# Performance work log

Measured on AMD Instinct MI355X. Metric: run time of the kernel, lower is better.

## Reference

```python
import jax, jax.numpy as jnp
import numpy as np

LAMBDA_SPATIAL = 1.0  # fixed buffer, not trained
GAMMA_ADJ = 1.0       # fixed buffer, not trained


def setup_inputs() -> dict:
    key = jax.random.key(0)
    k1, k2, k3, k4 = jax.random.split(key, 4)
    B, T, N, D = 8, 20, 512, 64
    h = jax.random.normal(k1, (B, T, N, D), dtype=jnp.float32)
    velocities = jax.random.normal(k2, (B, T, N, 2), dtype=jnp.float32)
    adjacency_weighted = jax.random.uniform(k3, (B, T, N, N), dtype=jnp.float32)
    node_mask = jax.random.randint(k4, (B, T, N), 0, 2).astype(bool)
    return {
        "h": h,
        "velocities": velocities,
        "adjacency_weighted": adjacency_weighted,
        "node_mask": node_mask,
    }


def reference(h, velocities, adjacency_weighted, node_mask):
    # h: [B,T,N,d]; velocities: [B,T,N,2]; adjacency_weighted: [B,T,N,N]; node_mask: [B,T,N]
    mask = node_mask.astype(bool)
    pair_m = mask[..., :, None] & mask[..., None, :]          # [B,T,N,N]

    # pairwise squared velocity distance, Eq. (3)
    dv = velocities[..., :, None, :] - velocities[..., None, :, :]  # [B,T,N,N,2]
    d2 = jnp.maximum(jnp.sum(dv * dv, axis=-1), 0.0)                # [B,T,N,N]

    logits_s = -LAMBDA_SPATIAL * d2 + GAMMA_ADJ * adjacency_weighted
    neg = jnp.finfo(logits_s.dtype).min
    logits_s = jnp.where(pair_m, logits_s, neg)
    row_ok = mask[..., :, None]
    logits_s = jnp.where(row_ok, logits_s, jnp.zeros_like(logits_s))

    alpha = jax.nn.softmax(logits_s, axis=-1)
    alpha = jnp.nan_to_num(alpha, nan=0.0, posinf=0.0, neginf=0.0)
    alpha = alpha / jnp.maximum(jnp.sum(alpha, axis=-1, keepdims=True), 1e-8)
    h_spatial = jnp.matmul(alpha, h)                          # [B,T,N,d]

    # temporal path: masked mean-pool over nodes, T x T similarity softmax
    mask_f = mask.astype(h.dtype)
    denom = jnp.maximum(jnp.sum(mask_f, axis=-1, keepdims=True), 1.0)  # [B,T,1]
    h_mean = jnp.sum(h * mask_f[..., None], axis=-2) / denom           # [B,T,d]
    m_b = jnp.matmul(h_mean, jnp.swapaxes(h_mean, -1, -2))             # [B,T,T]
    beta = jax.nn.softmax(m_b, axis=-1)
    h_temporal = jnp.einsum("btu,bund->btnd", beta, h)                 # [B,T,N,d]

    out = (h + h_spatial + h_temporal) * mask_f[..., None]
    return out
```

## Files before the change

kernel.cpp:

```cpp
#include <hip/hip_runtime.h>
#include <float.h>

#define BB 8
#define TT 20
#define NN 512
#define DD 64
#define BT (BB*TT)

typedef __bf16 bf16x8 __attribute__((ext_vector_type(8)));
typedef __bf16 bf16x4 __attribute__((ext_vector_type(4)));
typedef float f32x4 __attribute__((ext_vector_type(4)));

__global__ __launch_bounds__(256) void kpre(const float* __restrict__ h,
                                            const float* __restrict__ vel,
                                            const int* __restrict__ mask,
                                            __bf16* __restrict__ ht,
                                            __bf16* __restrict__ hb16,
                                            float* __restrict__ hpart,
                                            int* __restrict__ cpart,
                                            float4* __restrict__ colinfo,
                                            int* __restrict__ rows) {
    int bx = blockIdx.x;
    int bt = bx >> 3, slice = bx & 7;
    int n0 = slice * 64;
    int tid = threadIdx.x;
    const float* hp = h + ((size_t)bt * NN + n0) * DD;
    const int* mp = mask + (size_t)bt * NN + n0;
    short* htp = (short*)(ht + (size_t)bt * DD * NN) + n0;

    __shared__ __bf16 t[64][72];
    __shared__ float sred[16][64];

    int d4 = (tid & 15) << 2;
    int nl0 = tid >> 4;
    float s0 = 0.f, s1 = 0.f, s2 = 0.f, s3 = 0.f;
#pragma unroll
    for (int it = 0; it < 4; ++it) {
        int nl = it * 16 + nl0;
        float4 v = *(const float4*)(hp + (size_t)nl * DD + d4);
        if (mp[nl]) { s0 += v.x; s1 += v.y; s2 += v.z; s3 += v.w; }
        __bf16 b0 = (__bf16)v.x, b1 = (__bf16)v.y, b2 = (__bf16)v.z, b3 = (__bf16)v.w;
        t[d4 + 0][nl] = b0;
        t[d4 + 1][nl] = b1;
        t[d4 + 2][nl] = b2;
        t[d4 + 3][nl] = b3;
        bf16x4 pv = {b0, b1, b2, b3};
        *(bf16x4*)(hb16 + ((size_t)bt * NN + n0 + nl) * DD + d4) = pv;
    }
    int g = tid >> 4;
    sred[g][d4 + 0] = s0; sred[g][d4 + 1] = s1;
    sred[g][d4 + 2] = s2; sred[g][d4 + 3] = s3;
    __syncthreads();
#pragma unroll
    for (int it = 0; it < 4; ++it) {
        int idx = it * 256 + tid;
        int d = idx >> 4, s = idx & 15;
        short4 v4 = *(const short4*)&t[d][4 * s];
        *(short4*)(htp + (size_t)d * NN + 4 * s) = v4;
    }
    if (tid < 64) {
        float tot = 0.f;
#pragma unroll
        for (int k = 0; k < 16; ++k) tot += sred[k][tid];
        hpart[(size_t)bx * DD + tid] = tot;
    }
    if (tid < 64) {
        int j = n0 + tid;
        float2 v = ((const float2*)vel)[(size_t)bt * NN + j];
        int m = mp[tid];
        float cz = m ? -(v.x * v.x + v.y * v.y) : -3e38f;
        colinfo[(size_t)bt * NN + j] = make_float4(v.x, v.y, cz, 0.f);
        unsigned long long bal = __ballot(m != 0);
        int pos = __popcll(bal & ((1ull << tid) - 1ull));
        if (tid == 0) cpart[bx] = __popcll(bal);
        if (m) rows[(size_t)bt * NN + n0 + pos] = j;
    }
}

__global__ __launch_bounds__(256) void ktempbeta(const __bf16* __restrict__ hb16,
                                                 const int* __restrict__ mask,
                                                 const float* __restrict__ hpart,
                                                 const int* __restrict__ cpart,
                                                 float* __restrict__ out) {
    int b = blockIdx.x >> 5;
    int q4 = (blockIdx.x & 31) * 256 + threadIdx.x;
    int n = q4 >> 4;
    int tid = threadIdx.x;
    __shared__ float hm[TT][DD];
    __shared__ float mbuf[TT][TT];
    __shared__ float cf[TT][TT];
    __shared__ float invc[TT];
    if (tid < TT) {
        int c = 0;
#pragma unroll
        for (int k = 0; k < 8; ++k) c += cpart[(b * TT + tid) * 8 + k];
        invc[tid] = 1.f / fmaxf((float)c, 1.f);
    }
    __syncthreads();
    for (int idx = tid; idx < TT * DD; idx += 256) {
        int t = idx >> 6, d = idx & 63;
        const float* pp = hpart + ((size_t)(b * TT + t) * 8) * DD + d;
        float s = 0.f;
#pragma unroll
        for (int k = 0; k < 8; ++k) s += pp[k * DD];
        hm[t][d] = s * invc[t];
    }
    __syncthreads();
    for (int p = tid; p < TT * TT; p += 256) {
        int t = p / TT, u = p % TT;
        float s = 0.f;
        for (int d = 0; d < DD; ++d) s += hm[t][d] * hm[u][d];
        mbuf[t][u] = s;
    }
    __syncthreads();
    if (tid < TT) {
        float mx = -FLT_MAX;
        for (int u = 0; u < TT; ++u) mx = fmaxf(mx, mbuf[tid][u]);
        float e[TT]; float sum = 0.f;
        for (int u = 0; u < TT; ++u) { e[u] = __expf(mbuf[tid][u] - mx); sum += e[u]; }
        float inv = 1.f / sum;
        for (int u = 0; u < TT; ++u)
            cf[tid][u] = e[u] * inv + (tid == u ? 1.f : 0.f);
    }
    __syncthreads();
    const bf16x4* hp = (const bf16x4*)hb16 + (size_t)b * TT * 8192;
    float4* op = (float4*)out + (size_t)b * TT * 8192;
    const int* mp = mask + (size_t)b * TT * NN;
    float4 hv[TT];
#pragma unroll
    for (int u = 0; u < TT; ++u) {
        bf16x4 x = hp[(size_t)u * 8192 + q4];
        hv[u].x = (float)x[0]; hv[u].y = (float)x[1];
        hv[u].z = (float)x[2]; hv[u].w = (float)x[3];
    }
    float4 z = {0.f, 0.f, 0.f, 0.f};
#pragma unroll
    for (int t = 0; t < TT; ++t) {
        float4 a = z;
#pragma unroll
        for (int u = 0; u < TT; ++u) {
            float c = cf[t][u];
            a.x += c * hv[u].x; a.y += c * hv[u].y;
            a.z += c * hv[u].z; a.w += c * hv[u].w;
        }
        int m = mp[(size_t)t * NN + n];
        op[(size_t)t * 8192 + q4] = m ? a : z;
    }
}

__global__ __launch_bounds__(256) void kspatial(const float* __restrict__ adj,
                                                const float* __restrict__ vel,
                                                const int* __restrict__ cpart,
                                                const int* __restrict__ rows,
                                                const float4* __restrict__ colinfo,
                                                const __bf16* __restrict__ ht,
                                                float* __restrict__ out) {
    int bx = blockIdx.x;
    int x = bx & 7;
    int m8 = bx >> 3;
    int bt = x * 20 + (m8 >> 3);
    int i0 = (m8 & 7) * 64;

    const int* cp = cpart + bt * 8;
    int cs[8];
#pragma unroll
    for (int s = 0; s < 8; ++s) cs[s] = cp[s];
    int n_act = 0;
#pragma unroll
    for (int s = 0; s < 8; ++s) n_act += cs[s];
    if (i0 >= n_act) return;

    int tid = threadIdx.x;
    int w = tid >> 6, lane = tid & 63;
    int arow = lane & 15;
    int kg = lane >> 4;

    __shared__ __bf16 hs[64][520];
    __shared__ float4 ci[NN];

    for (int idx = tid; idx < NN; idx += 256)
        ci[idx] = colinfo[(size_t)bt * NN + idx];

    const ushort* htb = (const ushort*)(ht + (size_t)bt * DD * NN);
#pragma unroll
    for (int it = 0; it < 16; ++it) {
        int chunk = it * 256 + tid;
        int r = chunk >> 6;
        int cc = chunk & 63;
        *(uint4*)(&hs[r][cc * 8]) = *(const uint4*)(htb + (size_t)r * NN + cc * 8);
    }

    int slot = i0 + w * 16 + arow;
    int slotc = slot < n_act ? slot : n_act - 1;
    int row = 0, base = 0;
#pragma unroll
    for (int s = 0; s < 8; ++s) {
        if (slotc >= base && slotc < base + cs[s])
            row = rows[(size_t)bt * NN + s * 64 + (slotc - base)];
        base += cs[s];
    }
    float2 rv = ((const float2*)vel)[(size_t)bt * NN + row];
    float vx2 = 2.f * rv.x, vy2 = 2.f * rv.y;

    const float* arowp = adj + ((size_t)bt * NN + row) * NN;

    f32x4 zero = {0.f, 0.f, 0.f, 0.f};
    f32x4 acc[4];
#pragma unroll
    for (int nt = 0; nt < 4; ++nt) acc[nt] = zero;
    float lsum = 0.f;
    __syncthreads();

    f32x4 a01[16], a23[16];
    {
        const f32x4* p0 = (const f32x4*)(arowp + kg * 8);
        a01[0] = p0[0];
        a23[0] = p0[1];
        a01[1] = p0[8];
        a23[1] = p0[9];
    }
#pragma unroll
    for (int c = 0; c < 16; ++c) {
        if (c < 14) {
            const f32x4* pn = (const f32x4*)(arowp + kg * 8 + (c + 2) * 32);
            a01[c + 2] = pn[0];
            a23[c + 2] = pn[1];
        }
        int jb = kg * 8 + c * 32;
        const float4* ccp = &ci[jb];
        float p[8];
#pragma unroll
        for (int e = 0; e < 8; ++e) {
            float av = (e < 4) ? a01[c][e] : a23[c][e - 4];
            float4 cc = ccp[e];
            float l = av + cc.z + vx2 * cc.x + vy2 * cc.y;
            p[e] = __expf(l);
        }
        lsum += ((p[0] + p[1]) + (p[2] + p[3])) + ((p[4] + p[5]) + (p[6] + p[7]));
        bf16x8 af;
#pragma unroll
        for (int e = 0; e < 8; ++e) af[e] = (__bf16)p[e];
#pragma unroll
        for (int nt = 0; nt < 4; ++nt) {
            bf16x8 bf = *(const bf16x8*)(&hs[nt * 16 + arow][jb]);
            acc[nt] = __builtin_amdgcn_mfma_f32_16x16x32_bf16(af, bf, acc[nt], 0, 0, 0);
        }
    }

    lsum += __shfl_xor(lsum, 16, 64);
    lsum += __shfl_xor(lsum, 32, 64);
    float inv = 1.0f / fmaxf(lsum, 1e-8f);

    float* op = out + (size_t)bt * NN * DD;
#pragma unroll
    for (int q = 0; q < 4; ++q) {
        int cr = kg * 4 + q;
        int s2 = i0 + w * 16 + cr;
        int r2 = __shfl(row, cr, 64);
        float iv = __shfl(inv, cr, 64);
        if (s2 < n_act) {
#pragma unroll
            for (int nt = 0; nt < 4; ++nt) {
                size_t o = (size_t)r2 * DD + nt * 16 + arow;
                op[o] = op[o] + acc[nt][q] * iv;
            }
        }
    }
}

extern "C" void kernel_launch(void* const* d_in, const int* in_sizes, int n_in,
                              void* d_out, int out_size, void* d_ws, size_t ws_size,
                              hipStream_t stream) {
    const float* h   = (const float*)d_in[0];
    const float* vel = (const float*)d_in[1];
    const float* adj = (const float*)d_in[2];
    const int* mask  = (const int*)d_in[3];
    float* out = (float*)d_out;

    char* ws = (char*)d_ws;
    __bf16* ht      = (__bf16*)ws;                       ws += (size_t)BT * DD * NN * 2;
    __bf16* hb16    = (__bf16*)ws;                       ws += (size_t)BT * NN * DD * 2;
    float4* colinfo = (float4*)ws;                       ws += (size_t)BT * NN * 16;
    float* hpart    = (float*)ws;                        ws += (size_t)BT * 8 * DD * 4;
    int* cpart      = (int*)ws;                          ws += (size_t)BT * 8 * 4;
    int* rows       = (int*)ws;

    kpre<<<BT * 8, 256, 0, stream>>>(h, vel, mask, ht, hb16, hpart, cpart, colinfo, rows);
    ktempbeta<<<BB * 32, 256, 0, stream>>>(hb16, mask, hpart, cpart, out);
    kspatial<<<BT * 8, 256, 0, stream>>>(adj, vel, cpart, rows, colinfo, ht, out);
}
```

Baseline: 63.19 us.

## Halve kspatial LDS footprint with two-phase h staging and compact column info

The spatial kernel now stages the transposed h tile in two 256-column halves, so the shared buffer is about half its former size. Column info shrinks from float4 to float2: masked columns get a huge sentinel velocity, which drives the logit to a large negative value so exp gives zero. The adjacency prefetch drops from a full 16-chunk register array to a one-chunk lookahead, and launch bounds now ask for 4 blocks per CU. The aim is higher occupancy, traded against less in-flight memory parallelism per wave and two extra barriers.

```diff
diff --git a/kernel.cpp b/kernel.cpp
--- a/kernel.cpp
+++ b/kernel.cpp
@@ -18,7 +18,7 @@
                                             __bf16* __restrict__ hb16,
                                             float* __restrict__ hpart,
                                             int* __restrict__ cpart,
-                                            float4* __restrict__ colinfo,
+                                            float2* __restrict__ colinfo,
                                             int* __restrict__ rows) {
     int bx = blockIdx.x;
     int bt = bx >> 3, slice = bx & 7;
@@ -68,8 +68,10 @@
         int j = n0 + tid;
         float2 v = ((const float2*)vel)[(size_t)bt * NN + j];
         int m = mp[tid];
-        float cz = m ? -(v.x * v.x + v.y * v.y) : -3e38f;
-        colinfo[(size_t)bt * NN + j] = make_float4(v.x, v.y, cz, 0.f);
+        float2 cw;
+        cw.x = m ? v.x : 1e18f;
+        cw.y = m ? v.y : 1e18f;
+        colinfo[(size_t)bt * NN + j] = cw;
         unsigned long long bal = __ballot(m != 0);
         int pos = __popcll(bal & ((1ull << tid) - 1ull));
         if (tid == 0) cpart[bx] = __popcll(bal);
@@ -148,13 +150,13 @@
     }
 }
 
-__global__ __launch_bounds__(256) void kspatial(const float* __restrict__ adj,
-                                                const float* __restrict__ vel,
-                                                const int* __restrict__ cpart,
-                                                const int* __restrict__ rows,
-                                                const float4* __restrict__ colinfo,
-                                                const __bf16* __restrict__ ht,
-                                                float* __restrict__ out) {
+__global__ __launch_bounds__(256, 4) void kspatial(const float* __restrict__ adj,
+                                                   const float* __restrict__ vel,
+                                                   const int* __restrict__ cpart,
+                                                   const int* __restrict__ rows,
+                                                   const float2* __restrict__ colinfo,
+                                                   const __bf16* __restrict__ ht,
+                                                   float* __restrict__ out) {
     int bx = blockIdx.x;
     int x = bx & 7;
     int m8 = bx >> 3;
@@ -175,20 +177,11 @@
     int arow = lane & 15;
     int kg = lane >> 4;
 
-    __shared__ __bf16 hs[64][520];
-    __shared__ float4 ci[NN];
-
-    for (int idx = tid; idx < NN; idx += 256)
-        ci[idx] = colinfo[(size_t)bt * NN + idx];
-
-    const ushort* htb = (const ushort*)(ht + (size_t)bt * DD * NN);
-#pragma unroll
-    for (int it = 0; it < 16; ++it) {
-        int chunk = it * 256 + tid;
-        int r = chunk >> 6;
-        int cc = chunk & 63;
-        *(uint4*)(&hs[r][cc * 8]) = *(const uint4*)(htb + (size_t)r * NN + cc * 8);
-    }
+    __shared__ __bf16 hs[64][264];
+    __shared__ float2 vc[NN];
+
+    vc[tid] = colinfo[(size_t)bt * NN + tid];
+    vc[256 + tid] = colinfo[(size_t)bt * NN + 256 + tid];
 
     int slot = i0 + w * 16 + arow;
     int slotc = slot < n_act ? slot : n_act - 1;
@@ -203,47 +196,57 @@
     float vx2 = 2.f * rv.x, vy2 = 2.f * rv.y;
 
     const float* arowp = adj + ((size_t)bt * NN + row) * NN;
+    const ushort* htb = (const ushort*)(ht + (size_t)bt * DD * NN);
 
     f32x4 zero = {0.f, 0.f, 0.f, 0.f};
     f32x4 acc[4];
 #pragma unroll
     for (int nt = 0; nt < 4; ++nt) acc[nt] = zero;
     float lsum = 0.f;
-    __syncthreads();
-
-    f32x4 a01[16], a23[16];
-    {
-        const f32x4* p0 = (const f32x4*)(arowp + kg * 8);
-        a01[0] = p0[0];
-        a23[0] = p0[1];
-        a01[1] = p0[8];
-        a23[1] = p0[9];
-    }
-#pragma unroll
-    for (int c = 0; c < 16; ++c) {
-        if (c < 14) {
-            const f32x4* pn = (const f32x4*)(arowp + kg * 8 + (c + 2) * 32);
-            a01[c + 2] = pn[0];
-            a23[c + 2] = pn[1];
-        }
-        int jb = kg * 8 + c * 32;
-        const float4* ccp = &ci[jb];
-        float p[8];
-#pragma unroll
-        for (int e = 0; e < 8; ++e) {
-            float av = (e < 4) ? a01[c][e] : a23[c][e - 4];
-            float4 cc = ccp[e];
-            float l = av + cc.z + vx2 * cc.x + vy2 * cc.y;
-            p[e] = __expf(l);
-        }
-        lsum += ((p[0] + p[1]) + (p[2] + p[3])) + ((p[4] + p[5]) + (p[6] + p[7]));
-        bf16x8 af;
-#pragma unroll
-        for (int e = 0; e < 8; ++e) af[e] = (__bf16)p[e];
-#pragma unroll
-        for (int nt = 0; nt < 4; ++nt) {
-            bf16x8 bf = *(const bf16x8*)(&hs[nt * 16 + arow][jb]);
-            acc[nt] = __builtin_amdgcn_mfma_f32_16x16x32_bf16(af, bf, acc[nt], 0, 0, 0);
+
+#pragma unroll
+    for (int half = 0; half < 2; ++half) {
+        __syncthreads();
+        const ushort* src = htb + half * 256;
+#pragma unroll
+        for (int it = 0; it < 8; ++it) {
+            int chunk = it * 256 + tid;
+            int r = chunk >> 5;
+            int cc = chunk & 31;
+            *(uint4*)(&hs[r][cc * 8]) = *(const uint4*)(src + (size_t)r * NN + cc * 8);
+        }
+        __syncthreads();
+
+        const float* ap = arowp + half * 256;
+        const float2* vcp = &vc[half * 256];
+        f32x4 c01 = *(const f32x4*)(ap + kg * 8);
+        f32x4 c23 = *(const f32x4*)(ap + kg * 8 + 4);
+#pragma unroll
+        for (int c = 0; c < 8; ++c) {
+            f32x4 n01, n23;
+            if (c < 7) {
+                n01 = *(const f32x4*)(ap + kg * 8 + (c + 1) * 32);
+                n23 = *(const f32x4*)(ap + kg * 8 + (c + 1) * 32 + 4);
+            }
+            int jb = kg * 8 + c * 32;
+            float p[8];
+#pragma unroll
+            for (int e = 0; e < 8; ++e) {
+                float av = (e < 4) ? c01[e] : c23[e - 4];
+                float2 cc2 = vcp[jb + e];
+                float l = av + cc2.x * (vx2 - cc2.x) + cc2.y * (vy2 - cc2.y);
+                p[e] = __expf(l);
+            }
+            lsum += ((p[0] + p[1]) + (p[2] + p[3])) + ((p[4] + p[5]) + (p[6] + p[7]));
+            bf16x8 af;
+#pragma unroll
+            for (int e = 0; e < 8; ++e) af[e] = (__bf16)p[e];
+#pragma unroll
+            for (int nt = 0; nt < 4; ++nt) {
+                bf16x8 bf = *(const bf16x8*)(&hs[nt * 16 + arow][jb]);
+                acc[nt] = __builtin_amdgcn_mfma_f32_16x16x32_bf16(af, bf, acc[nt], 0, 0, 0);
+            }
+            c01 = n01; c23 = n23;
         }
     }
 
@@ -280,7 +283,7 @@
     char* ws = (char*)d_ws;
     __bf16* ht      = (__bf16*)ws;                       ws += (size_t)BT * DD * NN * 2;
     __bf16* hb16    = (__bf16*)ws;                       ws += (size_t)BT * NN * DD * 2;
-    float4* colinfo = (float4*)ws;                       ws += (size_t)BT * NN * 16;
+    float2* colinfo = (float2*)ws;                       ws += (size_t)BT * NN * 8;
     float* hpart    = (float*)ws;                        ws += (size_t)BT * 8 * DD * 4;
     int* cpart      = (int*)ws;                          ws += (size_t)BT * 8 * 4;
     int* rows       = (int*)ws;
```

Result: faster. 57.11 us (-9.6%).
